# Optimization experiments

Hardware: AMD Instinct MI355X
Metric: run time of the kernel (lower is better)

Reference implementation:

```python
import jax, jax.numpy as jnp
import numpy as np

NEG_INF = -1.0e9  # matches the source's close_to_negative_inf


def setup_inputs() -> dict:
    key = jax.random.key(0)
    k1, k2, k3, k4 = jax.random.split(key, 4)
    B, S, H, Dh = 2, 2048, 16, 64
    d_model = H * Dh
    return {
        "pre_q": jax.random.normal(k1, (B, S, H, Dh), dtype=jnp.float32),
        "pre_v": jax.random.normal(k2, (B, S, H, Dh), dtype=jnp.float32),
        "pre_k": jax.random.normal(k3, (B, S, H, Dh), dtype=jnp.float32),
        "output_weights": jax.random.normal(k4, (d_model, d_model), dtype=jnp.float32) * (1.0 / np.sqrt(d_model)),
        "out_seq_len": S,
        "d_model": d_model,
    }


def reference(pre_q, pre_v, pre_k, output_weights, out_seq_len, d_model):
    B, S, H, Dh = pre_q.shape
    # (B, H, S, Dh)
    q = jnp.transpose(pre_q, (0, 2, 1, 3))
    k = jnp.transpose(pre_k, (0, 2, 1, 3))
    v = jnp.transpose(pre_v, (0, 2, 1, 3))
    scale = 1.0 / jnp.sqrt(jnp.float32(Dh))
    # scaled QK^T: (B, H, Sq, Sk)
    scores = jnp.einsum("bhqd,bhkd->bhqk", q, k) * scale
    # source masking: multiply by lower triangle, add -1e9 on upper triangle
    tril = jnp.tril(jnp.ones((S, S), dtype=scores.dtype))
    masked = tril * scores + NEG_INF * (1.0 - tril)
    attn = jax.nn.softmax(masked, axis=-1)
    heads = jnp.einsum("bhqk,bhkd->bhqd", attn, v)  # (B, H, S, Dh)
    merged = jnp.transpose(heads, (0, 2, 1, 3)).reshape(B, S, H * Dh)
    out = jnp.einsum("bsd,de->bse", merged, output_weights)
    return out.reshape(-1, out_seq_len, d_model)
```

## Files before the change

### kernel.cpp

```cpp
#include <hip/hip_runtime.h>
#include <stdint.h>

#define S_LEN 2048
#define NH 16
#define DH 64
#define DM 1024

typedef __attribute__((ext_vector_type(8))) short short8;
typedef __attribute__((ext_vector_type(4))) float f32x4;

__device__ __forceinline__ unsigned short f2bf(float f) {
  union { float f; uint32_t u; } c; c.f = f;
  uint32_t u = c.u;
  return (unsigned short)((u + 0x7FFFu + ((u >> 16) & 1u)) >> 16);
}

__device__ __forceinline__ uint32_t pk_bf16(float lo, float hi) {
  uint32_t r;
  asm("v_cvt_pk_bf16_f32 %0, %1, %2" : "=v"(r) : "v"(lo), "v"(hi));
  return r;
}

__device__ __forceinline__ void g2l16(const void* g, void* l) {
  __builtin_amdgcn_global_load_lds(
      (const __attribute__((address_space(1))) uint32_t*)g,
      (__attribute__((address_space(3))) uint32_t*)l, 16, 0, 0);
}

#define PL32(a, b) asm("v_permlane32_swap_b32 %0, %1" : "+v"(a), "+v"(b))
#define PL16(a, b) asm("v_permlane16_swap_b32 %0, %1" : "+v"(a), "+v"(b))

__global__ __launch_bounds__(256) void prep_kernel(const float* __restrict__ K,
                                                   const float* __restrict__ V,
                                                   const float* __restrict__ W,
                                                   unsigned short* __restrict__ Kb,
                                                   unsigned short* __restrict__ Vt,
                                                   unsigned short* __restrict__ Wt) {
  __shared__ __align__(16) unsigned short tile[64 * 72];
  const int tid = threadIdx.x;
  const int blk = blockIdx.x;

  if (blk >= 1024) {
    const int wb = blk - 1024;
    const int e0 = (wb & 15) << 6;
    const int d0 = (wb >> 4) << 6;
#pragma unroll
    for (int i = 0; i < 4; ++i) {
      int idx = tid + i * 256;
      int d = idx >> 4;
      int ec = (idx & 15) << 2;
      float4 w = *(const float4*)(W + (size_t)(d0 + d) * DM + e0 + ec);
      tile[(ec + 0) * 72 + d] = f2bf(w.x);
      tile[(ec + 1) * 72 + d] = f2bf(w.y);
      tile[(ec + 2) * 72 + d] = f2bf(w.z);
      tile[(ec + 3) * 72 + d] = f2bf(w.w);
    }
    __syncthreads();
#pragma unroll
    for (int i = 0; i < 2; ++i) {
      int idx = tid + i * 256;
      int e = idx >> 3;
      int g = idx & 7;
      uint4 v = *(const uint4*)&tile[e * 72 + (g << 3)];
      *(uint4*)(Wt + (size_t)(e0 + e) * DM + d0 + ((g ^ (e & 7)) << 3)) = v;
    }
    return;
  }

  const int st = blk & 31;
  const int bh = blk >> 5;
  const int b = bh >> 4;
  const int h = bh & 15;
  const int s0 = st << 6;
  const size_t ibase = (size_t)b * (S_LEN * DM) + (size_t)h * DH;
  const size_t kbase = (size_t)bh * (S_LEN * DH);
  const size_t vbase = (size_t)bh * (DH * S_LEN);

#pragma unroll
  for (int i = 0; i < 4; ++i) {
    int idx = tid + i * 256;
    int s = idx >> 4;
    int d4 = (idx & 15) << 2;
    int g = d4 >> 3, rem = d4 & 7;
    float4 kv = *(const float4*)(K + ibase + (size_t)(s0 + s) * DM + d4);
    uint2 u;
    u.x = pk_bf16(kv.x, kv.y);
    u.y = pk_bf16(kv.z, kv.w);
    *(uint2*)(Kb + kbase + (size_t)(s0 + s) * DH + ((g ^ (s & 7)) << 3) + rem) = u;
  }
#pragma unroll
  for (int i = 0; i < 4; ++i) {
    int idx = tid + i * 256;
    int s = idx >> 4;
    int d4 = (idx & 15) << 2;
    float4 vv = *(const float4*)(V + ibase + (size_t)(s0 + s) * DM + d4);
    tile[(d4 + 0) * 72 + s] = f2bf(vv.x);
    tile[(d4 + 1) * 72 + s] = f2bf(vv.y);
    tile[(d4 + 2) * 72 + s] = f2bf(vv.z);
    tile[(d4 + 3) * 72 + s] = f2bf(vv.w);
  }
  __syncthreads();
#pragma unroll
  for (int i = 0; i < 2; ++i) {
    int idx = tid + i * 256;
    int d = idx >> 3;
    int g = idx & 7;
    uint4 u = *(const uint4*)&tile[d * 72 + (g << 3)];
    *(uint4*)(Vt + vbase + (size_t)d * S_LEN + s0 + ((g ^ (d & 7)) << 3)) = u;
  }
}

__global__ __launch_bounds__(256) void attn_kernel(const float* __restrict__ Q,
                                                   const unsigned short* __restrict__ Kb,
                                                   const unsigned short* __restrict__ Vt,
                                                   unsigned short* __restrict__ merged) {
  __shared__ __align__(16) unsigned short kbuf[2][64 * 64];
  __shared__ __align__(16) unsigned short vbuf[2][64 * 64];

  const int tid = threadIdx.x;
  const int wave = tid >> 6;
  const int lane = tid & 63;
  const int t = lane & 15;
  const int qd = lane >> 4;
  const int tx = t & 7;

  const int bid = blockIdx.x;
  const int bh = bid & 31;
  const int r = (bid >> 5) & 7;
  const int c = bid >> 8;
  const int qt = (c == 0) ? (31 - r) : (c == 1) ? (16 + r) : (c == 2) ? (15 - r) : r;
  const int h = bh & 15;
  const int b = bh >> 4;

  const int q0 = qt << 6;
  const int row0 = q0 + (wave << 4);
  const size_t qbase = (size_t)b * (S_LEN * DM) + (size_t)h * DH;
  const unsigned short* kg = Kb + (size_t)bh * (S_LEN * DH);
  const unsigned short* vg = Vt + (size_t)bh * (DH * S_LEN);

  short8 qfrag[2];
  {
    const float SC = 0.125f * 1.4426950408889634f;
    const float* qp = Q + qbase + (size_t)(row0 + t) * DM + (qd << 3);
#pragma unroll
    for (int kk = 0; kk < 2; ++kk) {
      float4 f0 = *(const float4*)(qp + kk * 32);
      float4 f1 = *(const float4*)(qp + kk * 32 + 4);
      union { short8 s; uint32_t u[4]; } qq;
      qq.u[0] = pk_bf16(f0.x * SC, f0.y * SC);
      qq.u[1] = pk_bf16(f0.z * SC, f0.w * SC);
      qq.u[2] = pk_bf16(f1.x * SC, f1.y * SC);
      qq.u[3] = pk_bf16(f1.z * SC, f1.w * SC);
      qfrag[kk] = qq.s;
    }
  }

  const int c1 = wave * 512;
  const int c2 = (wave + 4) * 512;
  const int l8 = lane * 8;
  auto stage = [&](int bsel, int kt0) {
    g2l16(kg + (size_t)kt0 * DH + c1 + l8, &kbuf[bsel][c1]);
    g2l16(kg + (size_t)kt0 * DH + c2 + l8, &kbuf[bsel][c2]);
    int o1 = c1 + l8, o2 = c2 + l8;
    g2l16(vg + (size_t)(o1 >> 6) * S_LEN + kt0 + (o1 & 63), &vbuf[bsel][c1]);
    g2l16(vg + (size_t)(o2 >> 6) * S_LEN + kt0 + (o2 & 63), &vbuf[bsel][c2]);
  };

  const f32x4 fzero = {0.f, 0.f, 0.f, 0.f};
  float lsum = 0.f;
  f32x4 o_acc[4];
#pragma unroll
  for (int nb = 0; nb < 4; ++nb) o_acc[nb] = fzero;

  const int ntiles = qt + 1;
  stage(0, 0);
  int cur = 0;

  for (int tile = 0; tile < ntiles; ++tile) {
    asm volatile("s_waitcnt vmcnt(0)" ::: "memory");
    __builtin_amdgcn_s_barrier();
    asm volatile("" ::: "memory");
    if (tile + 1 < ntiles) stage(cur ^ 1, (tile + 1) << 6);

    const unsigned short* kl = kbuf[cur];
    const unsigned short* vl = vbuf[cur];

    f32x4 sc[4];
#pragma unroll
    for (int cb = 0; cb < 4; ++cb) {
      const int row = cb * 16 + t;
      short8 a0 = *(const short8*)&kl[row * 64 + ((qd ^ tx) << 3)];
      short8 a1 = *(const short8*)&kl[row * 64 + (((4 | qd) ^ tx) << 3)];
      f32x4 a = fzero;
      a = __builtin_amdgcn_mfma_f32_16x16x32_bf16(a0, qfrag[0], a, 0, 0, 0);
      a = __builtin_amdgcn_mfma_f32_16x16x32_bf16(a1, qfrag[1], a, 0, 0, 0);
      sc[cb] = a;
    }

    if (tile == ntiles - 1) {
#pragma unroll
      for (int cb = 0; cb < 4; ++cb)
#pragma unroll
        for (int r2 = 0; r2 < 4; ++r2)
          if ((tile << 6) + cb * 16 + qd * 4 + r2 > row0 + t) sc[cb][r2] = -INFINITY;
    }

#pragma unroll
    for (int cb = 0; cb < 4; ++cb)
#pragma unroll
      for (int r2 = 0; r2 < 4; ++r2)
        sc[cb][r2] = __builtin_amdgcn_exp2f(sc[cb][r2]);
    lsum += ((sc[0][0] + sc[0][1]) + (sc[0][2] + sc[0][3])) +
            ((sc[1][0] + sc[1][1]) + (sc[1][2] + sc[1][3])) +
            ((sc[2][0] + sc[2][1]) + (sc[2][2] + sc[2][3])) +
            ((sc[3][0] + sc[3][1]) + (sc[3][2] + sc[3][3]));

    uint32_t p00 = pk_bf16(sc[0][0], sc[0][1]);
    uint32_t p01 = pk_bf16(sc[0][2], sc[0][3]);
    uint32_t p10 = pk_bf16(sc[1][0], sc[1][1]);
    uint32_t p11 = pk_bf16(sc[1][2], sc[1][3]);
    uint32_t p20 = pk_bf16(sc[2][0], sc[2][1]);
    uint32_t p21 = pk_bf16(sc[2][2], sc[2][3]);
    uint32_t p30 = pk_bf16(sc[3][0], sc[3][1]);
    uint32_t p31 = pk_bf16(sc[3][2], sc[3][3]);
    PL32(p00, p10); PL32(p01, p11);
    PL16(p00, p10); PL16(p01, p11);
    PL32(p20, p30); PL32(p21, p31);
    PL16(p20, p30); PL16(p21, p31);
    union { short8 s; uint32_t u[4]; } pa0, pa1;
    pa0.u[0] = p00; pa0.u[1] = p01; pa0.u[2] = p10; pa0.u[3] = p11;
    pa1.u[0] = p20; pa1.u[1] = p21; pa1.u[2] = p30; pa1.u[3] = p31;

#pragma unroll
    for (int nb = 0; nb < 4; ++nb) {
      short8 v0 = *(const short8*)&vl[(nb * 16 + t) * 64 + ((qd ^ tx) << 3)];
      o_acc[nb] = __builtin_amdgcn_mfma_f32_16x16x32_bf16(v0, pa0.s, o_acc[nb], 0, 0, 0);
      short8 v1 = *(const short8*)&vl[(nb * 16 + t) * 64 + (((4 | qd) ^ tx) << 3)];
      o_acc[nb] = __builtin_amdgcn_mfma_f32_16x16x32_bf16(v1, pa1.s, o_acc[nb], 0, 0, 0);
    }

    cur ^= 1;
  }

  lsum += __shfl_xor(lsum, 16);
  lsum += __shfl_xor(lsum, 32);
  const float invl = __builtin_amdgcn_rcpf(lsum);

  uint32_t e00 = pk_bf16(o_acc[0][0] * invl, o_acc[0][1] * invl);
  uint32_t e01 = pk_bf16(o_acc[0][2] * invl, o_acc[0][3] * invl);
  uint32_t e10 = pk_bf16(o_acc[1][0] * invl, o_acc[1][1] * invl);
  uint32_t e11 = pk_bf16(o_acc[1][2] * invl, o_acc[1][3] * invl);
  uint32_t e20 = pk_bf16(o_acc[2][0] * invl, o_acc[2][1] * invl);
  uint32_t e21 = pk_bf16(o_acc[2][2] * invl, o_acc[2][3] * invl);
  uint32_t e30 = pk_bf16(o_acc[3][0] * invl, o_acc[3][1] * invl);
  uint32_t e31 = pk_bf16(o_acc[3][2] * invl, o_acc[3][3] * invl);
  PL32(e00, e20); PL32(e10, e30);
  PL16(e00, e10); PL16(e20, e30);
  PL32(e01, e21); PL32(e11, e31);
  PL16(e01, e11); PL16(e21, e31);
  union { uint4 v; uint32_t u[4]; } u0, u1;
  u0.u[0] = e00; u0.u[1] = e01; u0.u[2] = e10; u0.u[3] = e11;
  u1.u[0] = e20; u1.u[1] = e21; u1.u[2] = e30; u1.u[3] = e31;
  unsigned short* mp = merged + (size_t)(b * S_LEN + row0 + t) * DM + h * DH;
  *(uint4*)(mp + (((2 * qd) ^ tx) << 3)) = u0.v;
  *(uint4*)(mp + (((2 * qd + 1) ^ tx) << 3)) = u1.v;
}

__global__ __launch_bounds__(256) void gemm_kernel(const unsigned short* __restrict__ A,
                                                   const unsigned short* __restrict__ Bt,
                                                   float* __restrict__ C) {
  __shared__ __align__(16) unsigned short abuf[2][128 * 64];
  __shared__ __align__(16) unsigned short bbuf[2][128 * 64];
  const int tid = threadIdx.x;
  const int wave = tid >> 6;
  const int lane = tid & 63;
  const int t = lane & 15;
  const int qd = lane >> 4;
  const int tx = t & 7;
  const int wm = wave >> 1;
  const int wn = wave & 1;
  const int n0 = blockIdx.x << 7;
  const int m0 = blockIdx.y << 7;

  const int rin = lane >> 3;
  const int cin = (lane & 7) << 3;
  auto stage = [&](int bsel, int kt) {
#pragma unroll
    for (int i = 0; i < 4; ++i) {
      int c = wave * 4 + i;
      int row = c * 8 + rin;
      g2l16(A + (size_t)(m0 + row) * DM + kt + cin, &abuf[bsel][c * 512]);
      g2l16(Bt + (size_t)(n0 + row) * DM + kt + cin, &bbuf[bsel][c * 512]);
    }
  };

  const f32x4 fzero = {0.f, 0.f, 0.f, 0.f};
  f32x4 acc[4][4];
#pragma unroll
  for (int mi = 0; mi < 4; ++mi)
#pragma unroll
    for (int nb = 0; nb < 4; ++nb) acc[mi][nb] = fzero;

  stage(0, 0);
  int cur = 0;

  for (int kt = 0; kt < DM; kt += 64) {
    asm volatile("s_waitcnt vmcnt(0)" ::: "memory");
    __builtin_amdgcn_s_barrier();
    asm volatile("" ::: "memory");
    if (kt + 64 < DM) stage(cur ^ 1, kt + 64);
    const unsigned short* al = abuf[cur];
    const unsigned short* bl = bbuf[cur];
#pragma unroll
    for (int kk = 0; kk < 2; ++kk) {
      const int sw = ((kk * 4 + qd) ^ tx) << 3;
      short8 af[4], bf[4];
#pragma unroll
      for (int mi = 0; mi < 4; ++mi)
        af[mi] = *(const short8*)&al[(wm * 64 + mi * 16 + t) * 64 + sw];
#pragma unroll
      for (int nb = 0; nb < 4; ++nb)
        bf[nb] = *(const short8*)&bl[(wn * 64 + nb * 16 + t) * 64 + sw];
#pragma unroll
      for (int mi = 0; mi < 4; ++mi)
#pragma unroll
        for (int nb = 0; nb < 4; ++nb)
          acc[mi][nb] = __builtin_amdgcn_mfma_f32_16x16x32_bf16(af[mi], bf[nb], acc[mi][nb], 0, 0, 0);
    }
    cur ^= 1;
  }
#pragma unroll
  for (int mi = 0; mi < 4; ++mi)
#pragma unroll
    for (int nb = 0; nb < 4; ++nb)
#pragma unroll
      for (int r = 0; r < 4; ++r)
        C[(size_t)(m0 + wm * 64 + mi * 16 + qd * 4 + r) * DM + n0 + wn * 64 + nb * 16 + t] =
            acc[mi][nb][r];
}

extern "C" void kernel_launch(void* const* d_in, const int* in_sizes, int n_in,
                              void* d_out, int out_size, void* d_ws, size_t ws_size,
                              hipStream_t stream) {
  const float* pre_q = (const float*)d_in[0];
  const float* pre_v = (const float*)d_in[1];
  const float* pre_k = (const float*)d_in[2];
  const float* W     = (const float*)d_in[3];
  float* out = (float*)d_out;

  unsigned short* Wt = (unsigned short*)d_ws;
  unsigned short* merged = Wt + (size_t)DM * DM;
  unsigned short* Kb = merged + (size_t)4096 * DM;
  unsigned short* Vt = Kb + (size_t)32 * S_LEN * DH;

  prep_kernel<<<dim3(1280), 256, 0, stream>>>(pre_k, pre_v, W, Kb, Vt, Wt);
  attn_kernel<<<dim3(1024), 256, 0, stream>>>(pre_q, Kb, Vt, merged);
  gemm_kernel<<<dim3(8, 32), 256, 0, stream>>>(merged, Wt, out);
}
```

Baseline: 155.7 us.

## Load K/V fragments directly from global memory instead of LDS double buffering

Removes the LDS double-buffered staging of K and V tiles. Each wave now reads its MFMA operand fragments straight from global memory into registers, relying on L1/L2 reuse across the four waves. The XOR swizzle in the K/V preprocessing layout is dropped to match. The q-tile block ordering is also simplified to a plain descending order in place of the interleaved balancing scheme. This removes barriers and LDS traffic, but each block now does 4x redundant global loads and has no prefetch overlap, so load latency is exposed.

New measurement: 263.8 us. 1.69x slower.

```diff
diff --git a/kernel.cpp b/kernel.cpp
--- a/kernel.cpp
+++ b/kernel.cpp
@@ -81,12 +81,11 @@
     int idx = tid + i * 256;
     int s = idx >> 4;
     int d4 = (idx & 15) << 2;
-    int g = d4 >> 3, rem = d4 & 7;
     float4 kv = *(const float4*)(K + ibase + (size_t)(s0 + s) * DM + d4);
     uint2 u;
     u.x = pk_bf16(kv.x, kv.y);
     u.y = pk_bf16(kv.z, kv.w);
-    *(uint2*)(Kb + kbase + (size_t)(s0 + s) * DH + ((g ^ (s & 7)) << 3) + rem) = u;
+    *(uint2*)(Kb + kbase + (size_t)(s0 + s) * DH + d4) = u;
   }
 #pragma unroll
   for (int i = 0; i < 4; ++i) {
@@ -106,7 +105,7 @@
     int d = idx >> 3;
     int g = idx & 7;
     uint4 u = *(const uint4*)&tile[d * 72 + (g << 3)];
-    *(uint4*)(Vt + vbase + (size_t)d * S_LEN + s0 + ((g ^ (d & 7)) << 3)) = u;
+    *(uint4*)(Vt + vbase + (size_t)d * S_LEN + s0 + (g << 3)) = u;
   }
 }
 
@@ -114,9 +113,6 @@
                                                    const unsigned short* __restrict__ Kb,
                                                    const unsigned short* __restrict__ Vt,
                                                    unsigned short* __restrict__ merged) {
-  __shared__ __align__(16) unsigned short kbuf[2][64 * 64];
-  __shared__ __align__(16) unsigned short vbuf[2][64 * 64];
-
   const int tid = threadIdx.x;
   const int wave = tid >> 6;
   const int lane = tid & 63;
@@ -125,10 +121,8 @@
   const int tx = t & 7;
 
   const int bid = blockIdx.x;
+  const int qt = 31 - (bid >> 5);
   const int bh = bid & 31;
-  const int r = (bid >> 5) & 7;
-  const int c = bid >> 8;
-  const int qt = (c == 0) ? (31 - r) : (c == 1) ? (16 + r) : (c == 2) ? (15 - r) : r;
   const int h = bh & 15;
   const int b = bh >> 4;
 
@@ -155,17 +149,6 @@
     }
   }
 
-  const int c1 = wave * 512;
-  const int c2 = (wave + 4) * 512;
-  const int l8 = lane * 8;
-  auto stage = [&](int bsel, int kt0) {
-    g2l16(kg + (size_t)kt0 * DH + c1 + l8, &kbuf[bsel][c1]);
-    g2l16(kg + (size_t)kt0 * DH + c2 + l8, &kbuf[bsel][c2]);
-    int o1 = c1 + l8, o2 = c2 + l8;
-    g2l16(vg + (size_t)(o1 >> 6) * S_LEN + kt0 + (o1 & 63), &vbuf[bsel][c1]);
-    g2l16(vg + (size_t)(o2 >> 6) * S_LEN + kt0 + (o2 & 63), &vbuf[bsel][c2]);
-  };
-
   const f32x4 fzero = {0.f, 0.f, 0.f, 0.f};
   float lsum = 0.f;
   f32x4 o_acc[4];
@@ -173,27 +156,29 @@
   for (int nb = 0; nb < 4; ++nb) o_acc[nb] = fzero;
 
   const int ntiles = qt + 1;
-  stage(0, 0);
-  int cur = 0;
-
   for (int tile = 0; tile < ntiles; ++tile) {
-    asm volatile("s_waitcnt vmcnt(0)" ::: "memory");
-    __builtin_amdgcn_s_barrier();
-    asm volatile("" ::: "memory");
-    if (tile + 1 < ntiles) stage(cur ^ 1, (tile + 1) << 6);
-
-    const unsigned short* kl = kbuf[cur];
-    const unsigned short* vl = vbuf[cur];
+    const int kt0 = tile << 6;
+
+    short8 ka[4][2], va[4][2];
+#pragma unroll
+    for (int cb = 0; cb < 4; ++cb) {
+      const unsigned short* kr = kg + (size_t)(kt0 + cb * 16 + t) * DH + (qd << 3);
+      ka[cb][0] = *(const short8*)(kr);
+      ka[cb][1] = *(const short8*)(kr + 32);
+    }
+#pragma unroll
+    for (int nb = 0; nb < 4; ++nb) {
+      const unsigned short* vr = vg + (size_t)(nb * 16 + t) * S_LEN + kt0 + (qd << 3);
+      va[nb][0] = *(const short8*)(vr);
+      va[nb][1] = *(const short8*)(vr + 32);
+    }
 
     f32x4 sc[4];
 #pragma unroll
     for (int cb = 0; cb < 4; ++cb) {
-      const int row = cb * 16 + t;
-      short8 a0 = *(const short8*)&kl[row * 64 + ((qd ^ tx) << 3)];
-      short8 a1 = *(const short8*)&kl[row * 64 + (((4 | qd) ^ tx) << 3)];
       f32x4 a = fzero;
-      a = __builtin_amdgcn_mfma_f32_16x16x32_bf16(a0, qfrag[0], a, 0, 0, 0);
-      a = __builtin_amdgcn_mfma_f32_16x16x32_bf16(a1, qfrag[1], a, 0, 0, 0);
+      a = __builtin_amdgcn_mfma_f32_16x16x32_bf16(ka[cb][0], qfrag[0], a, 0, 0, 0);
+      a = __builtin_amdgcn_mfma_f32_16x16x32_bf16(ka[cb][1], qfrag[1], a, 0, 0, 0);
       sc[cb] = a;
     }
 
@@ -202,7 +187,7 @@
       for (int cb = 0; cb < 4; ++cb)
 #pragma unroll
         for (int r2 = 0; r2 < 4; ++r2)
-          if ((tile << 6) + cb * 16 + qd * 4 + r2 > row0 + t) sc[cb][r2] = -INFINITY;
+          if (kt0 + cb * 16 + qd * 4 + r2 > row0 + t) sc[cb][r2] = -INFINITY;
     }
 
 #pragma unroll
@@ -233,13 +218,9 @@
 
 #pragma unroll
     for (int nb = 0; nb < 4; ++nb) {
-      short8 v0 = *(const short8*)&vl[(nb * 16 + t) * 64 + ((qd ^ tx) << 3)];
-      o_acc[nb] = __builtin_amdgcn_mfma_f32_16x16x32_bf16(v0, pa0.s, o_acc[nb], 0, 0, 0);
-      short8 v1 = *(const short8*)&vl[(nb * 16 + t) * 64 + (((4 | qd) ^ tx) << 3)];
-      o_acc[nb] = __builtin_amdgcn_mfma_f32_16x16x32_bf16(v1, pa1.s, o_acc[nb], 0, 0, 0);
-    }
-
-    cur ^= 1;
+      o_acc[nb] = __builtin_amdgcn_mfma_f32_16x16x32_bf16(va[nb][0], pa0.s, o_acc[nb], 0, 0, 0);
+      o_acc[nb] = __builtin_amdgcn_mfma_f32_16x16x32_bf16(va[nb][1], pa1.s, o_acc[nb], 0, 0, 0);
+    }
   }
 
   lsum += __shfl_xor(lsum, 16);
```
